# Optimization experiments

Measured on AMD Instinct MI355X. Metric: run time of the kernel, lower is better.

## Reference

```python
import jax, jax.numpy as jnp
import numpy as np

BETA = 0.9
THRESHOLD = 1.0
SURROGATE_K = 25.0  # superspike slope

@jax.custom_vjp
def spike(u):
    # Heaviside forward, superspike surrogate gradient
    return (u > 0).astype(u.dtype)

def _spike_fwd(u):
    return spike(u), u

def _spike_bwd(u, g):
    return (g / jnp.square(1.0 + SURROGATE_K * jnp.abs(u)),)

spike.defvjp(_spike_fwd, _spike_bwd)

T, B = 512, 256
VIS_D, IMU_D, TRAJ_D = 256, 64, 64
HID, OUT = 256, 128
FUSE = VIS_D + IMU_D + TRAJ_D  # 384

def setup_inputs() -> dict:
    key = jax.random.key(0)
    ks = jax.random.split(key, 8)
    s_in = 1.0 / np.sqrt(FUSE)
    s_h = 1.0 / np.sqrt(HID)
    return {
        "vis_seq": jax.random.normal(ks[0], (T, B, VIS_D), jnp.float32),
        "imu_seq": jax.random.normal(ks[1], (T, B, IMU_D), jnp.float32),
        "traj_seq": jax.random.normal(ks[2], (T, B, TRAJ_D), jnp.float32),
        "W_in": jax.random.normal(ks[3], (FUSE, HID), jnp.float32) * s_in,
        "b_in": jnp.zeros((HID,), jnp.float32),
        "w_rec": jax.random.normal(ks[4], (HID,), jnp.float32) * 0.1,  # RLIF elementwise recurrent weight
        "W_head": jax.random.normal(ks[5], (HID, OUT), jnp.float32) * s_h,
        "b_head": jnp.zeros((OUT,), jnp.float32),
    }

def reference(vis_seq, imu_seq, traj_seq, W_in, b_in, w_rec, W_head, b_head):
    # fuse latents: [T, B, FUSE]
    fuse_seq = jnp.concatenate([vis_seq, imu_seq, traj_seq], axis=-1)
    # in_proj is time-invariant -> hoist the GEMM out of the scan (same math)
    x_proj = jnp.einsum("tbf,fh->tbh", fuse_seq, W_in) + b_in  # [T, B, HID]
    batch = imu_seq.shape[1]
    V0 = jnp.zeros((batch, HID), x_proj.dtype)
    S0 = jnp.zeros((batch, HID), x_proj.dtype)

    def step(carry, x_t):
        V, S = carry
        # recurrent LIF: leak + input + elementwise recurrent spike feedback
        V = BETA * V + x_t + w_rec * S
        S_new = spike(V - THRESHOLD)
        V = V - S_new * THRESHOLD  # soft reset
        return (V, S_new), S_new

    _, spikes_seq = jax.lax.scan(step, (V0, S0), x_proj)  # [T, B, HID]
    # head is also time-invariant -> single GEMM over the whole sequence
    logits_seq = jnp.einsum("tbh,ho->tbo", spikes_seq, W_head) + b_head  # [T, B, OUT]
    out = jnp.mean(logits_seq, axis=0)  # readout='mean' over time
    return out, logits_seq
```

## Files before the change

### kernel.cpp

```cpp
#include <hip/hip_runtime.h>
#include <hip/hip_bf16.h>
#include <cstdint>

#define T_LEN 512
#define B_SZ  256
#define HID   256
#define OUT   128
#define FUSE  384
#define MROWS (T_LEN * B_SZ)
#define FT    64

typedef _Float16 f16x8 __attribute__((ext_vector_type(8)));
typedef float f32x4 __attribute__((ext_vector_type(4)));

#define PRESC 4096.0f
#define S1    2048.0f
#define S1INV 4.8828125e-4f
#define C0    5.9604644775390625e-8f

#define EPSV  5e-5f

__global__ __launch_bounds__(256) void prep_win(const float* __restrict__ Win,
                                                _Float16* __restrict__ Bpack)
{
  int id = blockIdx.x * 256 + threadIdx.x;
  int img = id >> 10;
  int c = img >> 1, bc = img & 1;
  int slot = id & 1023;
  int s = slot >> 9, sub = (slot >> 6) & 7, pos = slot & 63;
  int fr = pos & 15, fq = pos >> 4;
  int n = bc * 128 + sub * 16 + fr;
  int k0 = c * 32 + fq * 8;
  f16x8 v;
#pragma unroll
  for (int j = 0; j < 8; ++j) {
    float w = Win[(size_t)(k0 + j) * HID + n] * PRESC;
    _Float16 h = (_Float16)w;
    v[j] = (s == 0) ? h : (_Float16)((w - (float)h) * S1);
  }
  *reinterpret_cast<f16x8*>(&Bpack[(size_t)img * 8192 + slot * 8]) = v;
}

__global__ __launch_bounds__(256) void prep_whead(const float* __restrict__ Wh,
                                                  _Float16* __restrict__ Wh3)
{
  int id = blockIdx.x * 256 + threadIdx.x;
  int n = id & 127, kk = (id >> 7) & 31, c = id >> 12;
  Wh3[((size_t)c * 128 + n) * 32 + kk] = (_Float16)Wh[(c * 32 + kk) * OUT + n];
}

__global__ __launch_bounds__(512, 4) void k12_fused(
    const float* __restrict__ vis, const float* __restrict__ imu,
    const float* __restrict__ traj, const _Float16* __restrict__ Bpack,
    const float* __restrict__ bin, const float* __restrict__ wrec,
    uint32_t* __restrict__ sbits, float* __restrict__ scnt)
{
  __shared__ __align__(16) _Float16 Asl[4096];
  __shared__ float xt[FT][130];

  const int bid = blockIdx.x;
  const int b   = bid & 255;
  const int hh  = bid >> 8;
  const int tid = threadIdx.x;
  const int wid = tid >> 6, lane = tid & 63;
  const int wr = wid >> 2, wc = wid & 3;
  const int fr = lane & 15, fq = lane >> 4;

  const int arow = tid >> 2;
  const int ak   = (tid & 3) * 8;
  const int asub = arow >> 4;
  const int apos = (tid & 3) * 16 + (arow & 15);

  float V = 0.f, S = 0.f, cnt = 0.f, minm = 1e9f;
  const float wrv = (tid < 128) ? wrec[hh * 128 + tid] : 0.f;
  float bvv[2];
  bvv[0] = bin[hh * 128 + wc * 32 + fr];
  bvv[1] = bin[hh * 128 + wc * 32 + 16 + fr];

  float4 a0, a1;
  f16x8 pb0, pb1, pb2, pb3;

  auto loadA = [&](int tc, int c) {
    if (tid < 256) {
      size_t m = (size_t)(tc * FT + arow) * B_SZ + b;
      const float* src; size_t off;
      if (c < 8)       { src = vis;  off = m * 256 + c * 32 + ak; }
      else if (c < 10) { src = imu;  off = m * 64 + (c - 8) * 32 + ak; }
      else             { src = traj; off = m * 64 + (c - 10) * 32 + ak; }
      a0 = *reinterpret_cast<const float4*>(src + off);
      a1 = *reinterpret_cast<const float4*>(src + off + 4);
    }
  };
  auto loadB = [&](int c) {
    const _Float16* base = Bpack + (size_t)(c * 2 + hh) * 8192;
    pb0 = *reinterpret_cast<const f16x8*>(base + (wc * 2 + 0) * 512 + lane * 8);
    pb1 = *reinterpret_cast<const f16x8*>(base + (wc * 2 + 1) * 512 + lane * 8);
    pb2 = *reinterpret_cast<const f16x8*>(base + 4096 + (wc * 2 + 0) * 512 + lane * 8);
    pb3 = *reinterpret_cast<const f16x8*>(base + 4096 + (wc * 2 + 1) * 512 + lane * 8);
  };

  loadA(0, 0); loadB(0);

  for (int tc = 0; tc < 8; ++tc) {
    f32x4 acc0[2][2] = {};
    f32x4 acc1[2][2] = {};

#pragma unroll 1
    for (int c = 0; c < 12; ++c) {
      __syncthreads();
      if (tid < 256) {
        float av[8] = {a0.x, a0.y, a0.z, a0.w, a1.x, a1.y, a1.z, a1.w};
        f16x8 vh, vl;
#pragma unroll
        for (int j = 0; j < 8; ++j) {
          float w = av[j] * PRESC;
          _Float16 h = (_Float16)w;
          vh[j] = h;
          vl[j] = (_Float16)((w - (float)h) * S1);
        }
        *reinterpret_cast<f16x8*>(&Asl[asub * 512 + apos * 8])        = vh;
        *reinterpret_cast<f16x8*>(&Asl[2048 + asub * 512 + apos * 8]) = vl;
      }
      __syncthreads();
      f16x8 bh_0 = pb0, bh_1 = pb1, bl_0 = pb2, bl_1 = pb3;
      if (c + 1 < 12)      { loadA(tc, c + 1); loadB(c + 1); }
      else if (tc + 1 < 8) { loadA(tc + 1, 0); loadB(0); }

#pragma unroll
      for (int mf = 0; mf < 2; ++mf) {
        int sa = wr * 2 + mf;
        f16x8 ah = *reinterpret_cast<const f16x8*>(&Asl[sa * 512 + lane * 8]);
        f16x8 al = *reinterpret_cast<const f16x8*>(&Asl[2048 + sa * 512 + lane * 8]);
        acc0[mf][0] = __builtin_amdgcn_mfma_f32_16x16x32_f16(ah, bh_0, acc0[mf][0], 0, 0, 0);
        acc1[mf][0] = __builtin_amdgcn_mfma_f32_16x16x32_f16(ah, bl_0, acc1[mf][0], 0, 0, 0);
        acc1[mf][0] = __builtin_amdgcn_mfma_f32_16x16x32_f16(al, bh_0, acc1[mf][0], 0, 0, 0);
        acc0[mf][1] = __builtin_amdgcn_mfma_f32_16x16x32_f16(ah, bh_1, acc0[mf][1], 0, 0, 0);
        acc1[mf][1] = __builtin_amdgcn_mfma_f32_16x16x32_f16(ah, bl_1, acc1[mf][1], 0, 0, 0);
        acc1[mf][1] = __builtin_amdgcn_mfma_f32_16x16x32_f16(al, bh_1, acc1[mf][1], 0, 0, 0);
      }
    }

#pragma unroll
    for (int mf = 0; mf < 2; ++mf)
#pragma unroll
      for (int nf = 0; nf < 2; ++nf) {
        int col = wc * 32 + nf * 16 + fr;
        int rbase = wr * 32 + mf * 16 + fq * 4;
#pragma unroll
        for (int r = 0; r < 4; ++r)
          xt[rbase + r][col] =
              (acc0[mf][nf][r] + acc1[mf][nf][r] * S1INV) * C0 + bvv[nf];
      }
    __syncthreads();

    if (tid < 128) {
#pragma unroll 1
      for (int u0 = 0; u0 < FT; u0 += 8) {
        float xv[8];
#pragma unroll
        for (int u = 0; u < 8; ++u) xv[u] = xt[u0 + u][tid];
#pragma unroll
        for (int u = 0; u < 8; ++u) {
          V = 0.9f * V + xv[u] + wrv * S;
          float d = V - 1.0f;
          float sn = (d > 0.0f) ? 1.0f : 0.0f;
          minm = fminf(minm, fabsf(d));
          V -= sn;
          cnt += sn;
          S = sn;
          unsigned long long mk = __ballot(sn > 0.5f);
          if (lane == 0) {
            int m = (tc * FT + u0 + u) * B_SZ + b;
            int wv = hh * 2 + wid;
            sbits[(size_t)m * 8 + wv * 2 + 0] = (uint32_t)(mk & 0xffffffffull);
            sbits[(size_t)m * 8 + wv * 2 + 1] = (uint32_t)(mk >> 32);
          }
        }
      }
    }
  }

  if (tid < 128)
    scnt[b * HID + hh * 128 + tid] = (minm < EPSV) ? (-cnt - 1.0f) : cnt;
}

#define FSL 12
__global__ __launch_bounds__(512) void k2_fix(
    const float* __restrict__ vis, const float* __restrict__ imu,
    const float* __restrict__ traj, const float* __restrict__ Win,
    const float* __restrict__ bin, const float* __restrict__ wrec,
    uint32_t* __restrict__ sbits, float* __restrict__ scnt)
{
  __shared__ __align__(16) float Wlds[FSL][392];
  __shared__ float xcol[FSL][521];
  __shared__ unsigned char spkb[FSL][516];
  __shared__ int dlist[256];
  __shared__ int nd;

  const int b = blockIdx.x;
  const int tid = threadIdx.x;
  if (tid == 0) nd = 0;
  __syncthreads();
  if (tid < 256) {
    if (scnt[b * HID + tid] < -0.5f) {
      int p = atomicAdd(&nd, 1);
      dlist[p] = tid;
    }
  }
  __syncthreads();
  const int nd0 = nd;
  if (nd0 == 0) return;

  const int t = tid;
  const size_t r = (size_t)t * B_SZ + b;

  for (int sb = 0; sb < nd0; sb += FSL) {
    const int nsb = min(FSL, nd0 - sb);

    for (int idx = tid; idx < FSL * 384; idx += 512) {
      int s = idx / 384, k = idx - s * 384;
      float w = 0.f;
      if (s < nsb) w = Win[(size_t)k * HID + dlist[sb + s]];
      Wlds[s][k] = w;
    }
    __syncthreads();

    float x[FSL];
#pragma unroll
    for (int s = 0; s < FSL; ++s) x[s] = 0.f;

#define SEG(SRC, LEN, DIM, WOFS)                                              \
    {                                                                         \
      const float* src = SRC + r * DIM;                                       \
      _Pragma("unroll 1")                                                     \
      for (int q = 0; q < LEN; q += 4) {                                      \
        float4 a0 = *reinterpret_cast<const float4*>(src + q * 4);            \
        float4 a1 = *reinterpret_cast<const float4*>(src + q * 4 + 4);        \
        float4 a2 = *reinterpret_cast<const float4*>(src + q * 4 + 8);        \
        float4 a3 = *reinterpret_cast<const float4*>(src + q * 4 + 12);       \
        _Pragma("unroll")                                                     \
        for (int s = 0; s < FSL; ++s) {                                       \
          float4 w = *reinterpret_cast<const float4*>(&Wlds[s][WOFS + q * 4]);\
          x[s] += a0.x * w.x; x[s] += a0.y * w.y;                             \
          x[s] += a0.z * w.z; x[s] += a0.w * w.w;                             \
        }                                                                     \
        _Pragma("unroll")                                                     \
        for (int s = 0; s < FSL; ++s) {                                       \
          float4 w = *reinterpret_cast<const float4*>(&Wlds[s][WOFS + q * 4 + 4]); \
          x[s] += a1.x * w.x; x[s] += a1.y * w.y;                             \
          x[s] += a1.z * w.z; x[s] += a1.w * w.w;                             \
        }                                                                     \
        _Pragma("unroll")                                                     \
        for (int s = 0; s < FSL; ++s) {                                       \
          float4 w = *reinterpret_cast<const float4*>(&Wlds[s][WOFS + q * 4 + 8]); \
          x[s] += a2.x * w.x; x[s] += a2.y * w.y;                             \
          x[s] += a2.z * w.z; x[s] += a2.w * w.w;                             \
        }                                                                     \
        _Pragma("unroll")                                                     \
        for (int s = 0; s < FSL; ++s) {                                       \
          float4 w = *reinterpret_cast<const float4*>(&Wlds[s][WOFS + q * 4 + 12]); \
          x[s] += a3.x * w.x; x[s] += a3.y * w.y;                             \
          x[s] += a3.z * w.z; x[s] += a3.w * w.w;                             \
        }                                                                     \
      }                                                                       \
    }

    SEG(vis,  64, 256, 0)
    SEG(imu,  16, 64,  256)
    SEG(traj, 16, 64,  320)
#undef SEG

#pragma unroll
    for (int s = 0; s < FSL; ++s) {
      if (s < nsb) xcol[s][t] = x[s] + bin[dlist[sb + s]];
    }
    __syncthreads();

    if (tid < nsb) {
      const int h = dlist[sb + tid];
      const float mywr = wrec[h];
      float V = 0.f, Sv = 0.f, cnt = 0.f;
#pragma unroll 1
      for (int tt = 0; tt < T_LEN; ++tt) {
        float xv = xcol[tid][tt];
        V = 0.9f * V + xv + mywr * Sv;
        float sn = (V - 1.0f > 0.0f) ? 1.0f : 0.0f;
        V -= sn;
        cnt += sn;
        Sv = sn;
        spkb[tid][tt] = (unsigned char)sn;
      }
      scnt[b * HID + h] = cnt;
    }
    __syncthreads();

    for (int p = tid; p < T_LEN * 8; p += 512) {
      int tt = p >> 3, wv = p & 7;
      uint32_t mc = 0, ms = 0;
      for (int j = 0; j < nsb; ++j) {
        int h = dlist[sb + j];
        if ((h >> 5) == wv) {
          uint32_t bit = 1u << (h & 31);
          mc |= bit;
          if (spkb[j][tt]) ms |= bit;
        }
      }
      if (mc) {
        size_t w = ((size_t)tt * B_SZ + b) * 8 + wv;
        sbits[w] = (sbits[w] & ~mc) | ms;
      }
    }
    __syncthreads();
  }
}

#define LDA 40
__global__ __launch_bounds__(256) void k3_logits(
    const uint32_t* __restrict__ sbits, const _Float16* __restrict__ Wh3,
    const float* __restrict__ bhead, float* __restrict__ logits)
{
  __shared__ __align__(16) _Float16 Sa[128][LDA];
  __shared__ __align__(16) _Float16 Wt[128][LDA];

  const int tid  = threadIdx.x;
  const int brow = blockIdx.x * 128;
  const int srow = tid >> 1, sks = (tid & 1) << 4;
  const int wid = tid >> 6, lane = tid & 63;
  const int wr = wid >> 1, wc = wid & 1;
  const int fr = lane & 15, fq = lane >> 4;

  f32x4 acc[4][4] = {};
  uint32_t wbits;
  uint4 wb0, wb1;

  auto loadS = [&](int c) { wbits = sbits[(size_t)(brow + srow) * 8 + c]; };
  auto loadW = [&](int c) {
    const _Float16* p = Wh3 + ((size_t)c * 128 + srow) * 32 + sks;
    wb0 = *reinterpret_cast<const uint4*>(p);
    wb1 = *reinterpret_cast<const uint4*>(p + 8);
  };

  loadS(0); loadW(0);

  for (int c = 0; c < 8; ++c) {
    __syncthreads();
    {
      f16x8 e0, e1;
#pragma unroll
      for (int j = 0; j < 8; ++j) {
        e0[j] = (_Float16)(float)((wbits >> (sks + j)) & 1u);
        e1[j] = (_Float16)(float)((wbits >> (sks + 8 + j)) & 1u);
      }
      *reinterpret_cast<f16x8*>(&Sa[srow][sks])     = e0;
      *reinterpret_cast<f16x8*>(&Sa[srow][sks + 8]) = e1;
    }
    *reinterpret_cast<uint4*>(&Wt[srow][sks])     = wb0;
    *reinterpret_cast<uint4*>(&Wt[srow][sks + 8]) = wb1;
    __syncthreads();
    if (c + 1 < 8) { loadS(c + 1); loadW(c + 1); }

    f16x8 wf[4];
#pragma unroll
    for (int nf = 0; nf < 4; ++nf)
      wf[nf] = *reinterpret_cast<const f16x8*>(&Wt[wc * 64 + nf * 16 + fr][fq * 8]);
#pragma unroll
    for (int mf = 0; mf < 4; ++mf) {
      f16x8 sf = *reinterpret_cast<const f16x8*>(&Sa[wr * 64 + mf * 16 + fr][fq * 8]);
#pragma unroll
      for (int nf = 0; nf < 4; ++nf)
        acc[mf][nf] = __builtin_amdgcn_mfma_f32_16x16x32_f16(sf, wf[nf], acc[mf][nf], 0, 0, 0);
    }
  }

#pragma unroll
  for (int mf = 0; mf < 4; ++mf)
#pragma unroll
    for (int nf = 0; nf < 4; ++nf) {
      int n = wc * 64 + nf * 16 + fr;
      float bv = bhead[n];
#pragma unroll
      for (int r = 0; r < 4; ++r) {
        int m = brow + wr * 64 + mf * 16 + fq * 4 + r;
        logits[(size_t)m * OUT + n] = acc[mf][nf][r] + bv;
      }
    }
}

__global__ __launch_bounds__(128) void k4_out(
    const float* __restrict__ scnt, const float* __restrict__ Whead,
    const float* __restrict__ bhead, float* __restrict__ outp)
{
  __shared__ float s[HID];
  const int b = blockIdx.x;
  const int o = threadIdx.x;
  s[o] = scnt[b * HID + o];
  s[o + 128] = scnt[b * HID + o + 128];
  __syncthreads();
  float acc = 0.f;
#pragma unroll 8
  for (int h = 0; h < HID; ++h) acc += s[h] * Whead[h * OUT + o];
  outp[b * OUT + o] = acc * (1.0f / (float)T_LEN) + bhead[o];
}

extern "C" void kernel_launch(void* const* d_in, const int* in_sizes, int n_in,
                              void* d_out, int out_size, void* d_ws, size_t ws_size,
                              hipStream_t stream)
{
  const float* vis   = (const float*)d_in[0];
  const float* imu   = (const float*)d_in[1];
  const float* traj  = (const float*)d_in[2];
  const float* Win   = (const float*)d_in[3];
  const float* bin   = (const float*)d_in[4];
  const float* wrec  = (const float*)d_in[5];
  const float* Whead = (const float*)d_in[6];
  const float* bhead = (const float*)d_in[7];

  float* outp   = (float*)d_out;
  float* logits = outp + B_SZ * OUT;

  char* ws = (char*)d_ws;
  const size_t SBITS_B = (size_t)MROWS * 8 * 4;
  const size_t SCNT_B  = (size_t)B_SZ * HID * 4;
  const size_t BPACK_B = (size_t)24 * 8192 * 2;
  uint32_t* sbits = (uint32_t*)ws;
  float*    scnt  = (float*)(ws + SBITS_B);
  _Float16* Bpack = (_Float16*)(ws + SBITS_B + SCNT_B);
  _Float16* Wh3   = (_Float16*)(ws + SBITS_B + SCNT_B + BPACK_B);

  prep_win  <<<dim3(24576 / 256), 256, 0, stream>>>(Win, Bpack);
  prep_whead<<<dim3(32768 / 256), 256, 0, stream>>>(Whead, Wh3);
  k12_fused <<<dim3(512),         512, 0, stream>>>(vis, imu, traj, Bpack, bin,
                                                    wrec, sbits, scnt);
  k2_fix    <<<dim3(B_SZ),        512, 0, stream>>>(vis, imu, traj, Win, bin,
                                                    wrec, sbits, scnt);
  k3_logits <<<dim3(MROWS / 128), 256, 0, stream>>>(sbits, Wh3, bhead, logits);
  k4_out    <<<dim3(B_SZ),        128, 0, stream>>>(scnt, Whead, bhead, outp);
}
```

Measured before the change: 274.1 us.

## Merge prep kernels and restructure logits GEMM with fragment-ordered LDS and register weights

Merges the two weight-prep kernels into a single launch to save one kernel launch. Reworks the logits GEMM to 512 threads per block over 256 rows. Spike bits are unpacked straight into LDS in MFMA fragment order, so each lane reads its A fragment contiguously without padding. Head-weight fragments now load from global memory into registers instead of being staged through LDS, which removes one LDS copy but raises register pressure and repeats global weight loads across waves.

Result: slower. 296.2 us (+8.1%).

```diff
diff --git a/kernel.cpp b/kernel.cpp
--- a/kernel.cpp
+++ b/kernel.cpp
@@ -20,33 +20,34 @@
 
 #define EPSV  5e-5f
 
-__global__ __launch_bounds__(256) void prep_win(const float* __restrict__ Win,
-                                                _Float16* __restrict__ Bpack)
-{
-  int id = blockIdx.x * 256 + threadIdx.x;
-  int img = id >> 10;
-  int c = img >> 1, bc = img & 1;
-  int slot = id & 1023;
-  int s = slot >> 9, sub = (slot >> 6) & 7, pos = slot & 63;
-  int fr = pos & 15, fq = pos >> 4;
-  int n = bc * 128 + sub * 16 + fr;
-  int k0 = c * 32 + fq * 8;
-  f16x8 v;
-#pragma unroll
-  for (int j = 0; j < 8; ++j) {
-    float w = Win[(size_t)(k0 + j) * HID + n] * PRESC;
-    _Float16 h = (_Float16)w;
-    v[j] = (s == 0) ? h : (_Float16)((w - (float)h) * S1);
+__global__ __launch_bounds__(256) void prep_all(const float* __restrict__ Win,
+                                                const float* __restrict__ Wh,
+                                                _Float16* __restrict__ Bpack,
+                                                _Float16* __restrict__ Wh3)
+{
+  int gid = blockIdx.x;
+  if (gid < 96) {
+    int id = gid * 256 + threadIdx.x;
+    int img = id >> 10;
+    int c = img >> 1, bc = img & 1;
+    int slot = id & 1023;
+    int s = slot >> 9, sub = (slot >> 6) & 7, pos = slot & 63;
+    int fr = pos & 15, fq = pos >> 4;
+    int n = bc * 128 + sub * 16 + fr;
+    int k0 = c * 32 + fq * 8;
+    f16x8 v;
+#pragma unroll
+    for (int j = 0; j < 8; ++j) {
+      float w = Win[(size_t)(k0 + j) * HID + n] * PRESC;
+      _Float16 h = (_Float16)w;
+      v[j] = (s == 0) ? h : (_Float16)((w - (float)h) * S1);
+    }
+    *reinterpret_cast<f16x8*>(&Bpack[(size_t)img * 8192 + slot * 8]) = v;
+  } else {
+    int id = (gid - 96) * 256 + threadIdx.x;
+    int n = id & 127, kk = (id >> 7) & 31, c = id >> 12;
+    Wh3[((size_t)c * 128 + n) * 32 + kk] = (_Float16)Wh[(c * 32 + kk) * OUT + n];
   }
-  *reinterpret_cast<f16x8*>(&Bpack[(size_t)img * 8192 + slot * 8]) = v;
-}
-
-__global__ __launch_bounds__(256) void prep_whead(const float* __restrict__ Wh,
-                                                  _Float16* __restrict__ Wh3)
-{
-  int id = blockIdx.x * 256 + threadIdx.x;
-  int n = id & 127, kk = (id >> 7) & 31, c = id >> 12;
-  Wh3[((size_t)c * 128 + n) * 32 + kk] = (_Float16)Wh[(c * 32 + kk) * OUT + n];
 }
 
 __global__ __launch_bounds__(512, 4) void k12_fused(
@@ -314,61 +315,64 @@
   }
 }
 
-#define LDA 40
-__global__ __launch_bounds__(256) void k3_logits(
+__global__ __launch_bounds__(512, 4) void k3_logits(
     const uint32_t* __restrict__ sbits, const _Float16* __restrict__ Wh3,
     const float* __restrict__ bhead, float* __restrict__ logits)
 {
-  __shared__ __align__(16) _Float16 Sa[128][LDA];
-  __shared__ __align__(16) _Float16 Wt[128][LDA];
+  __shared__ __align__(16) _Float16 Sa[16384];
 
   const int tid  = threadIdx.x;
-  const int brow = blockIdx.x * 128;
-  const int srow = tid >> 1, sks = (tid & 1) << 4;
+  const int brow = blockIdx.x * 256;
   const int wid = tid >> 6, lane = tid & 63;
   const int wr = wid >> 1, wc = wid & 1;
   const int fr = lane & 15, fq = lane >> 4;
 
   f32x4 acc[4][4] = {};
-  uint32_t wbits;
-  uint4 wb0, wb1;
-
-  auto loadS = [&](int c) { wbits = sbits[(size_t)(brow + srow) * 8 + c]; };
+  uint32_t wbits[2];
+  f16x8 wf[4];
+
+  auto loadS = [&](int c) {
+#pragma unroll
+    for (int s2 = 0; s2 < 2; ++s2) {
+      int s = tid + s2 * 512;
+      int row = (s >> 6) * 16 + (s & 15);
+      wbits[s2] = sbits[(size_t)(brow + row) * 8 + c];
+    }
+  };
   auto loadW = [&](int c) {
-    const _Float16* p = Wh3 + ((size_t)c * 128 + srow) * 32 + sks;
-    wb0 = *reinterpret_cast<const uint4*>(p);
-    wb1 = *reinterpret_cast<const uint4*>(p + 8);
+#pragma unroll
+    for (int nf = 0; nf < 4; ++nf) {
+      int n = wc * 64 + nf * 16 + fr;
+      wf[nf] = *reinterpret_cast<const f16x8*>(Wh3 + ((size_t)c * 128 + n) * 32 + fq * 8);
+    }
   };
 
   loadS(0); loadW(0);
 
   for (int c = 0; c < 8; ++c) {
     __syncthreads();
-    {
-      f16x8 e0, e1;
-#pragma unroll
-      for (int j = 0; j < 8; ++j) {
-        e0[j] = (_Float16)(float)((wbits >> (sks + j)) & 1u);
-        e1[j] = (_Float16)(float)((wbits >> (sks + 8 + j)) & 1u);
-      }
-      *reinterpret_cast<f16x8*>(&Sa[srow][sks])     = e0;
-      *reinterpret_cast<f16x8*>(&Sa[srow][sks + 8]) = e1;
-    }
-    *reinterpret_cast<uint4*>(&Wt[srow][sks])     = wb0;
-    *reinterpret_cast<uint4*>(&Wt[srow][sks + 8]) = wb1;
-    __syncthreads();
+#pragma unroll
+    for (int s2 = 0; s2 < 2; ++s2) {
+      int s = tid + s2 * 512;
+      int kbase = ((s >> 4) & 3) * 8;
+      f16x8 e;
+#pragma unroll
+      for (int j = 0; j < 8; ++j)
+        e[j] = (_Float16)(float)((wbits[s2] >> (kbase + j)) & 1u);
+      *reinterpret_cast<f16x8*>(&Sa[s * 8]) = e;
+    }
+    __syncthreads();
+    f16x8 w0 = wf[0], w1 = wf[1], w2 = wf[2], w3 = wf[3];
     if (c + 1 < 8) { loadS(c + 1); loadW(c + 1); }
 
-    f16x8 wf[4];
-#pragma unroll
-    for (int nf = 0; nf < 4; ++nf)
-      wf[nf] = *reinterpret_cast<const f16x8*>(&Wt[wc * 64 + nf * 16 + fr][fq * 8]);
 #pragma unroll
     for (int mf = 0; mf < 4; ++mf) {
-      f16x8 sf = *reinterpret_cast<const f16x8*>(&Sa[wr * 64 + mf * 16 + fr][fq * 8]);
-#pragma unroll
-      for (int nf = 0; nf < 4; ++nf)
-        acc[mf][nf] = __builtin_amdgcn_mfma_f32_16x16x32_f16(sf, wf[nf], acc[mf][nf], 0, 0, 0);
+      int sa = wr * 4 + mf;
+      f16x8 sf = *reinterpret_cast<const f16x8*>(&Sa[(sa * 64 + lane) * 8]);
+      acc[mf][0] = __builtin_amdgcn_mfma_f32_16x16x32_f16(sf, w0, acc[mf][0], 0, 0, 0);
+      acc[mf][1] = __builtin_amdgcn_mfma_f32_16x16x32_f16(sf, w1, acc[mf][1], 0, 0, 0);
+      acc[mf][2] = __builtin_amdgcn_mfma_f32_16x16x32_f16(sf, w2, acc[mf][2], 0, 0, 0);
+      acc[mf][3] = __builtin_amdgcn_mfma_f32_16x16x32_f16(sf, w3, acc[mf][3], 0, 0, 0);
     }
   }
 
@@ -427,12 +431,11 @@
   _Float16* Bpack = (_Float16*)(ws + SBITS_B + SCNT_B);
   _Float16* Wh3   = (_Float16*)(ws + SBITS_B + SCNT_B + BPACK_B);
 
-  prep_win  <<<dim3(24576 / 256), 256, 0, stream>>>(Win, Bpack);
-  prep_whead<<<dim3(32768 / 256), 256, 0, stream>>>(Whead, Wh3);
+  prep_all  <<<dim3(224),         256, 0, stream>>>(Win, Whead, Bpack, Wh3);
   k12_fused <<<dim3(512),         512, 0, stream>>>(vis, imu, traj, Bpack, bin,
                                                     wrec, sbits, scnt);
   k2_fix    <<<dim3(B_SZ),        512, 0, stream>>>(vis, imu, traj, Win, bin,
                                                     wrec, sbits, scnt);
-  k3_logits <<<dim3(MROWS / 128), 256, 0, stream>>>(sbits, Wh3, bhead, logits);
+  k3_logits <<<dim3(MROWS / 256), 512, 0, stream>>>(sbits, Wh3, bhead, logits);
   k4_out    <<<dim3(B_SZ),        128, 0, stream>>>(scnt, Whead, bhead, outp);
 }
```

## Split recurrent hidden units across four blocks per batch and merge prep kernels

Applied to the files above, without the earlier changes.

The fused projection+LIF kernel now gives each block 64 hidden units instead of 128, so it launches 1024 blocks. This halves the MFMA work and accumulator registers per block, and the occupancy hint rises to 8. Each block's sequential scan is done by a single wave, and spreading the serial scan over more blocks aims to improve latency hiding. The cost is that every input tile is now loaded and split into fp16 four times instead of twice, which increases global or cache traffic. The two weight-prep kernels are also merged into one launch to save launch overhead.

Result: slower. 370.9 us (+35.3%).

```diff
diff --git a/kernel.cpp b/kernel.cpp
--- a/kernel.cpp
+++ b/kernel.cpp
@@ -20,43 +20,44 @@
 
 #define EPSV  5e-5f
 
-__global__ __launch_bounds__(256) void prep_win(const float* __restrict__ Win,
-                                                _Float16* __restrict__ Bpack)
-{
-  int id = blockIdx.x * 256 + threadIdx.x;
-  int img = id >> 10;
-  int c = img >> 1, bc = img & 1;
-  int slot = id & 1023;
-  int s = slot >> 9, sub = (slot >> 6) & 7, pos = slot & 63;
-  int fr = pos & 15, fq = pos >> 4;
-  int n = bc * 128 + sub * 16 + fr;
-  int k0 = c * 32 + fq * 8;
-  f16x8 v;
-#pragma unroll
-  for (int j = 0; j < 8; ++j) {
-    float w = Win[(size_t)(k0 + j) * HID + n] * PRESC;
-    _Float16 h = (_Float16)w;
-    v[j] = (s == 0) ? h : (_Float16)((w - (float)h) * S1);
+__global__ __launch_bounds__(256) void prep_all(const float* __restrict__ Win,
+                                                const float* __restrict__ Wh,
+                                                _Float16* __restrict__ Bpack,
+                                                _Float16* __restrict__ Wh3)
+{
+  int gid = blockIdx.x;
+  if (gid < 96) {
+    int id = gid * 256 + threadIdx.x;
+    int img = id >> 10;
+    int c = img >> 1, bc = img & 1;
+    int slot = id & 1023;
+    int s = slot >> 9, sub = (slot >> 6) & 7, pos = slot & 63;
+    int fr = pos & 15, fq = pos >> 4;
+    int n = bc * 128 + sub * 16 + fr;
+    int k0 = c * 32 + fq * 8;
+    f16x8 v;
+#pragma unroll
+    for (int j = 0; j < 8; ++j) {
+      float w = Win[(size_t)(k0 + j) * HID + n] * PRESC;
+      _Float16 h = (_Float16)w;
+      v[j] = (s == 0) ? h : (_Float16)((w - (float)h) * S1);
+    }
+    *reinterpret_cast<f16x8*>(&Bpack[(size_t)img * 8192 + slot * 8]) = v;
+  } else {
+    int id = (gid - 96) * 256 + threadIdx.x;
+    int n = id & 127, kk = (id >> 7) & 31, c = id >> 12;
+    Wh3[((size_t)c * 128 + n) * 32 + kk] = (_Float16)Wh[(c * 32 + kk) * OUT + n];
   }
-  *reinterpret_cast<f16x8*>(&Bpack[(size_t)img * 8192 + slot * 8]) = v;
-}
-
-__global__ __launch_bounds__(256) void prep_whead(const float* __restrict__ Wh,
-                                                  _Float16* __restrict__ Wh3)
-{
-  int id = blockIdx.x * 256 + threadIdx.x;
-  int n = id & 127, kk = (id >> 7) & 31, c = id >> 12;
-  Wh3[((size_t)c * 128 + n) * 32 + kk] = (_Float16)Wh[(c * 32 + kk) * OUT + n];
-}
-
-__global__ __launch_bounds__(512, 4) void k12_fused(
+}
+
+__global__ __launch_bounds__(512, 8) void k12_fused(
     const float* __restrict__ vis, const float* __restrict__ imu,
     const float* __restrict__ traj, const _Float16* __restrict__ Bpack,
     const float* __restrict__ bin, const float* __restrict__ wrec,
     uint32_t* __restrict__ sbits, float* __restrict__ scnt)
 {
   __shared__ __align__(16) _Float16 Asl[4096];
-  __shared__ float xt[FT][130];
+  __shared__ float xt[FT][66];
 
   const int bid = blockIdx.x;
   const int b   = bid & 255;
@@ -72,13 +73,11 @@
   const int apos = (tid & 3) * 16 + (arow & 15);
 
   float V = 0.f, S = 0.f, cnt = 0.f, minm = 1e9f;
-  const float wrv = (tid < 128) ? wrec[hh * 128 + tid] : 0.f;
-  float bvv[2];
-  bvv[0] = bin[hh * 128 + wc * 32 + fr];
-  bvv[1] = bin[hh * 128 + wc * 32 + 16 + fr];
+  const float wrv = (tid < 64) ? wrec[hh * 64 + tid] : 0.f;
+  const float bv = bin[hh * 64 + wc * 16 + fr];
 
   float4 a0, a1;
-  f16x8 pb0, pb1, pb2, pb3;
+  f16x8 pbh, pbl;
 
   auto loadA = [&](int tc, int c) {
     if (tid < 256) {
@@ -92,18 +91,17 @@
     }
   };
   auto loadB = [&](int c) {
-    const _Float16* base = Bpack + (size_t)(c * 2 + hh) * 8192;
-    pb0 = *reinterpret_cast<const f16x8*>(base + (wc * 2 + 0) * 512 + lane * 8);
-    pb1 = *reinterpret_cast<const f16x8*>(base + (wc * 2 + 1) * 512 + lane * 8);
-    pb2 = *reinterpret_cast<const f16x8*>(base + 4096 + (wc * 2 + 0) * 512 + lane * 8);
-    pb3 = *reinterpret_cast<const f16x8*>(base + 4096 + (wc * 2 + 1) * 512 + lane * 8);
+    const _Float16* base = Bpack + (size_t)(c * 2 + (hh >> 1)) * 8192;
+    int sub = (hh & 1) * 4 + wc;
+    pbh = *reinterpret_cast<const f16x8*>(base + sub * 512 + lane * 8);
+    pbl = *reinterpret_cast<const f16x8*>(base + 4096 + sub * 512 + lane * 8);
   };
 
   loadA(0, 0); loadB(0);
 
   for (int tc = 0; tc < 8; ++tc) {
-    f32x4 acc0[2][2] = {};
-    f32x4 acc1[2][2] = {};
+    f32x4 acc0[2] = {};
+    f32x4 acc1[2] = {};
 
 #pragma unroll 1
     for (int c = 0; c < 12; ++c) {
@@ -122,7 +120,7 @@
         *reinterpret_cast<f16x8*>(&Asl[2048 + asub * 512 + apos * 8]) = vl;
       }
       __syncthreads();
-      f16x8 bh_0 = pb0, bh_1 = pb1, bl_0 = pb2, bl_1 = pb3;
+      f16x8 bh = pbh, bl = pbl;
       if (c + 1 < 12)      { loadA(tc, c + 1); loadB(c + 1); }
       else if (tc + 1 < 8) { loadA(tc + 1, 0); loadB(0); }
 
@@ -131,29 +129,23 @@
         int sa = wr * 2 + mf;
         f16x8 ah = *reinterpret_cast<const f16x8*>(&Asl[sa * 512 + lane * 8]);
         f16x8 al = *reinterpret_cast<const f16x8*>(&Asl[2048 + sa * 512 + lane * 8]);
-        acc0[mf][0] = __builtin_amdgcn_mfma_f32_16x16x32_f16(ah, bh_0, acc0[mf][0], 0, 0, 0);
-        acc1[mf][0] = __builtin_amdgcn_mfma_f32_16x16x32_f16(ah, bl_0, acc1[mf][0], 0, 0, 0);
-        acc1[mf][0] = __builtin_amdgcn_mfma_f32_16x16x32_f16(al, bh_0, acc1[mf][0], 0, 0, 0);
-        acc0[mf][1] = __builtin_amdgcn_mfma_f32_16x16x32_f16(ah, bh_1, acc0[mf][1], 0, 0, 0);
-        acc1[mf][1] = __builtin_amdgcn_mfma_f32_16x16x32_f16(ah, bl_1, acc1[mf][1], 0, 0, 0);
-        acc1[mf][1] = __builtin_amdgcn_mfma_f32_16x16x32_f16(al, bh_1, acc1[mf][1], 0, 0, 0);
-      }
-    }
-
-#pragma unroll
-    for (int mf = 0; mf < 2; ++mf)
-#pragma unroll
-      for (int nf = 0; nf < 2; ++nf) {
-        int col = wc * 32 + nf * 16 + fr;
-        int rbase = wr * 32 + mf * 16 + fq * 4;
-#pragma unroll
-        for (int r = 0; r < 4; ++r)
-          xt[rbase + r][col] =
-              (acc0[mf][nf][r] + acc1[mf][nf][r] * S1INV) * C0 + bvv[nf];
-      }
-    __syncthreads();
-
-    if (tid < 128) {
+        acc0[mf] = __builtin_amdgcn_mfma_f32_16x16x32_f16(ah, bh, acc0[mf], 0, 0, 0);
+        acc1[mf] = __builtin_amdgcn_mfma_f32_16x16x32_f16(ah, bl, acc1[mf], 0, 0, 0);
+        acc1[mf] = __builtin_amdgcn_mfma_f32_16x16x32_f16(al, bh, acc1[mf], 0, 0, 0);
+      }
+    }
+
+#pragma unroll
+    for (int mf = 0; mf < 2; ++mf) {
+      int col = wc * 16 + fr;
+      int rbase = wr * 32 + mf * 16 + fq * 4;
+#pragma unroll
+      for (int r = 0; r < 4; ++r)
+        xt[rbase + r][col] = (acc0[mf][r] + acc1[mf][r] * S1INV) * C0 + bv;
+    }
+    __syncthreads();
+
+    if (tid < 64) {
 #pragma unroll 1
       for (int u0 = 0; u0 < FT; u0 += 8) {
         float xv[8];
@@ -171,17 +163,16 @@
           unsigned long long mk = __ballot(sn > 0.5f);
           if (lane == 0) {
             int m = (tc * FT + u0 + u) * B_SZ + b;
-            int wv = hh * 2 + wid;
-            sbits[(size_t)m * 8 + wv * 2 + 0] = (uint32_t)(mk & 0xffffffffull);
-            sbits[(size_t)m * 8 + wv * 2 + 1] = (uint32_t)(mk >> 32);
+            sbits[(size_t)m * 8 + hh * 2 + 0] = (uint32_t)(mk & 0xffffffffull);
+            sbits[(size_t)m * 8 + hh * 2 + 1] = (uint32_t)(mk >> 32);
           }
         }
       }
     }
   }
 
-  if (tid < 128)
-    scnt[b * HID + hh * 128 + tid] = (minm < EPSV) ? (-cnt - 1.0f) : cnt;
+  if (tid < 64)
+    scnt[b * HID + hh * 64 + tid] = (minm < EPSV) ? (-cnt - 1.0f) : cnt;
 }
 
 #define FSL 12
@@ -427,9 +418,8 @@
   _Float16* Bpack = (_Float16*)(ws + SBITS_B + SCNT_B);
   _Float16* Wh3   = (_Float16*)(ws + SBITS_B + SCNT_B + BPACK_B);
 
-  prep_win  <<<dim3(24576 / 256), 256, 0, stream>>>(Win, Bpack);
-  prep_whead<<<dim3(32768 / 256), 256, 0, stream>>>(Whead, Wh3);
-  k12_fused <<<dim3(512),         512, 0, stream>>>(vis, imu, traj, Bpack, bin,
+  prep_all  <<<dim3(224),         256, 0, stream>>>(Win, Whead, Bpack, Wh3);
+  k12_fused <<<dim3(1024),        512, 0, stream>>>(vis, imu, traj, Bpack, bin,
                                                     wrec, sbits, scnt);
   k2_fix    <<<dim3(B_SZ),        512, 0, stream>>>(vis, imu, traj, Win, bin,
                                                     wrec, sbits, scnt);
```
